# Kernel tuning notes

Hardware: AMD Instinct MI355X
Metric: run time of the kernel (lower is better)

## Reference

```python
import jax, jax.numpy as jnp
import numpy as np

B_SZ, T, D_IN, D_STATE, D_OUT = 32, 4096, 128, 128, 128


def setup_inputs() -> dict:
    key = jax.random.key(0)
    k1, k2, k3, k4, k5 = jax.random.split(key, 5)
    inputs = jax.random.normal(k1, (B_SZ, T, D_IN), dtype=jnp.float32)
    # A ~ orthogonal initializer scaled to spectral radius 0.9 for a stable recurrence
    Araw = jax.random.normal(k2, (D_STATE, D_STATE), dtype=jnp.float32)
    Q, _ = jnp.linalg.qr(Araw)
    A = 0.9 * Q
    B = jax.random.normal(k3, (D_STATE, D_IN), dtype=jnp.float32) / np.sqrt(D_IN)
    C = jax.random.normal(k4, (D_OUT, D_STATE), dtype=jnp.float32) / np.sqrt(D_STATE)
    D = jax.random.normal(k5, (D_OUT, D_IN), dtype=jnp.float32) / np.sqrt(D_IN)
    return {"inputs": inputs, "A": A, "B": B, "C": C, "D": D}


def reference(inputs, A, B, C, D):
    """x(t+1) = A x(t) + B u(t);  y(t+1) = C x(t+1) + D u(t).
    x0 = 0, return_sequences=True -> output [batch, time, d_out]."""
    x0 = jnp.zeros((inputs.shape[0], A.shape[0]), dtype=inputs.dtype)
    u_tb = jnp.swapaxes(inputs, 0, 1)  # [T, batch, d_in]

    def step(x, u):
        x1 = x @ A.T + u @ B.T          # [batch, d_state]
        y1 = x1 @ C.T + u @ D.T         # [batch, d_out]
        return x1, y1

    _, ys = jax.lax.scan(step, x0, u_tb)
    return jnp.swapaxes(ys, 0, 1)       # [batch, T, d_out]
```

## Files before the change

### kernel.cpp

```cpp
#include <hip/hip_runtime.h>
#include <cstddef>
#include <cstdint>

#define DIM 128
#define T_LEN 4096
#define BATCH 32
#define L_CH 32
#define N_CH 128
#define N_CHAINS 4096
#define KFULL 4096

typedef float f32x4 __attribute__((ext_vector_type(4)));
typedef short s16x8 __attribute__((ext_vector_type(8)));
typedef unsigned short u16x4 __attribute__((ext_vector_type(4)));
typedef unsigned short u16x8 __attribute__((ext_vector_type(8)));
typedef unsigned int u32;

#define OFF_UBF  0
#define OFF_A64  8388608
#define OFF_A96  8404992
#define OFF_A128 8421376
#define OFF_VBF  8437760
#define OFF_MCBF 8716288
#define OFF_SBF  12582912
#define OFF_KBF  12845056
#define OFF_CABF 13107200
#define OFF_WBF  13377536
#define OFF_AP   13639680
#define OFF_CA   14180352
#define OFF_K    14704640
#define OFF_W    15228928
#define OFF_B    15753216
#define OFF_C    15769600
#define OFF_D    15785984
#define AP(d)    (OFF_AP + (d) * 16384)

__device__ __forceinline__ f32x4 ld_pin(const float* p) {
    return *reinterpret_cast<const volatile f32x4*>(p);
}
__device__ __forceinline__ unsigned short f2bf(float x) {
    u32 u = __builtin_bit_cast(u32, x);
    return (unsigned short)((u + 0x7FFFu + ((u >> 16) & 1u)) >> 16);
}
__device__ __forceinline__ void gld16(const void* g, void* l) {
    __builtin_amdgcn_global_load_lds((const __attribute__((address_space(1))) u32*)g,
                                     (__attribute__((address_space(3))) u32*)l, 16, 0, 0);
}

__global__ void k_init(const float* __restrict__ u, const float* __restrict__ A,
                       const float* __restrict__ B, const float* __restrict__ C,
                       const float* __restrict__ D, float* __restrict__ wsf) {
    if (blockIdx.x < 8192) {
        unsigned short* ubf = (unsigned short*)(wsf + OFF_UBF);
        const size_t e0 = (size_t)(blockIdx.x * 256 + threadIdx.x) * 8;
        const f32x4 v0 = *reinterpret_cast<const f32x4*>(u + e0);
        const f32x4 v1 = *reinterpret_cast<const f32x4*>(u + e0 + 4);
        u16x8 o;
        o[0] = f2bf(v0.x); o[1] = f2bf(v0.y); o[2] = f2bf(v0.z); o[3] = f2bf(v0.w);
        o[4] = f2bf(v1.x); o[5] = f2bf(v1.y); o[6] = f2bf(v1.z); o[7] = f2bf(v1.w);
        *reinterpret_cast<u16x8*>(ubf + e0) = o;
    } else {
        const int e0 = ((blockIdx.x - 8192) * 256 + threadIdx.x) * 4;
        const int mat = e0 >> 14, rem = e0 & 16383;
        const float* src = (mat == 0) ? A : (mat == 1) ? B : (mat == 2) ? C : D;
        const int dst = (mat == 0) ? AP(1) : (mat == 1) ? OFF_B : (mat == 2) ? OFF_C : OFF_D;
        *reinterpret_cast<f32x4*>(wsf + dst + rem) =
            *reinterpret_cast<const f32x4*>(src + rem);
    }
}

__global__ void k_castmats(float* __restrict__ wsf) {
    const int e0 = (blockIdx.x * 256 + threadIdx.x) * 4;
    unsigned short* KBF  = (unsigned short*)(wsf + OFF_KBF);
    unsigned short* CABF = (unsigned short*)(wsf + OFF_CABF);
    unsigned short* WBF  = (unsigned short*)(wsf + OFF_WBF);
    unsigned short* MCBF = (unsigned short*)(wsf + OFF_MCBF);
    u16x4 o;
    unsigned short* dst;
    if (e0 < 524288) {
        const f32x4 v = *reinterpret_cast<const f32x4*>(wsf + OFF_K + e0);
        o[0] = f2bf(v.x); o[1] = f2bf(v.y); o[2] = f2bf(v.z); o[3] = f2bf(v.w);
        dst = KBF + e0;
    } else if (e0 < 1048576) {
        const int i2 = e0 - 524288;
        const f32x4 v = *reinterpret_cast<const f32x4*>(wsf + OFF_CA + i2);
        o[0] = f2bf(v.x); o[1] = f2bf(v.y); o[2] = f2bf(v.z); o[3] = f2bf(v.w);
        dst = CABF + 16384 + i2;
    } else if (e0 < 1572864) {
        const int widx = e0 - 1048576;
        const int i = widx >> 12, j = (widx >> 7) & 31, kp = widx & 127;
        const int srco = (j == 31) ? (OFF_B + i * 128 + kp)
                                   : (OFF_W + j * 16384 + i * 128 + kp);
        const f32x4 v = *reinterpret_cast<const f32x4*>(wsf + srco);
        o[0] = f2bf(v.x); o[1] = f2bf(v.y); o[2] = f2bf(v.z); o[3] = f2bf(v.w);
        dst = WBF + widx;
    } else {
        const int mloc = e0 - 1572864;
        const int irow = mloc / 640;
        const int rem  = mloc - irow * 640;
        const int e    = rem >> 7;
        const int k    = rem & 127;
        if (e == 0) {
#pragma unroll
            for (int j = 0; j < 4; ++j)
                o[j] = (k + j == irow) ? (unsigned short)0x3F80 : (unsigned short)0;
        } else {
            const int moff = (e == 1) ? AP(32) : (e == 2) ? OFF_A64
                           : (e == 3) ? OFF_A96 : OFF_A128;
            const f32x4 v = *reinterpret_cast<const f32x4*>(wsf + moff + irow * 128 + k);
            o[0] = f2bf(v.x); o[1] = f2bf(v.y); o[2] = f2bf(v.z); o[3] = f2bf(v.w);
        }
        dst = MCBF + mloc;
    }
    *reinterpret_cast<u16x4*>(dst) = o;
}

struct MMDesc { int n; int xo[64]; int yo[64]; int oo[64]; int ao[64]; };

__global__ __launch_bounds__(256, 1) void k_mmb(float* __restrict__ wsf, MMDesc d) {
    const int mm = blockIdx.x >> 2, sub = blockIdx.x & 3;
    const float* X = wsf + d.xo[mm];
    const float* Y = wsf + d.yo[mm];
    float* O = wsf + d.oo[mm];
    const int ao = d.ao[mm];
    __shared__ __align__(16) float Ys[DIM][DIM];
    const int t = threadIdx.x;
#pragma unroll
    for (int i = 0; i < 16; ++i) {
        const int j = t + i * 256;
        reinterpret_cast<f32x4*>(&Ys[0][0])[j] = reinterpret_cast<const f32x4*>(Y)[j];
    }
    const int r = sub * 32 + (t >> 3);
    const int c0 = (t & 7) * 16;
    f32x4 xr[32];
#pragma unroll
    for (int k = 0; k < 32; ++k) xr[k] = ld_pin(&X[r * DIM + 4 * k]);
    __syncthreads();
    float acc[16];
#pragma unroll
    for (int j = 0; j < 16; ++j) acc[j] = 0.f;
#pragma unroll
    for (int k = 0; k < DIM; ++k) {
        const float xv = ((const float*)xr)[k];
#pragma unroll
        for (int j = 0; j < 16; j += 4) {
            const f32x4 yv = *reinterpret_cast<const f32x4*>(&Ys[k][c0 + j]);
            acc[j + 0] = fmaf(xv, yv.x, acc[j + 0]);
            acc[j + 1] = fmaf(xv, yv.y, acc[j + 1]);
            acc[j + 2] = fmaf(xv, yv.z, acc[j + 2]);
            acc[j + 3] = fmaf(xv, yv.w, acc[j + 3]);
        }
    }
    if (ao >= 0) {
        const float* Ad = wsf + ao;
#pragma unroll
        for (int j = 0; j < 16; ++j) acc[j] += Ad[r * DIM + c0 + j];
    }
#pragma unroll
    for (int j = 0; j < 16; j += 4) {
        f32x4 o; o.x = acc[j]; o.y = acc[j + 1]; o.z = acc[j + 2]; o.w = acc[j + 3];
        *reinterpret_cast<f32x4*>(&O[r * DIM + c0 + j]) = o;
    }
}

__global__ __launch_bounds__(256, 2) void k_gemm1(const unsigned short* __restrict__ UBF,
                                                  const unsigned short* __restrict__ WBF,
                                                  unsigned short* __restrict__ VBF) {
    __shared__ __align__(16) unsigned short lsA[2][4096];
    __shared__ __align__(16) unsigned short lsB[2][4096];
    const int b = blockIdx.x;
    const int t = threadIdx.x, w = t >> 6, l = t & 63;
    const int wr = w >> 1, wc = w & 1;
    const int m0 = b * 128;
    const int rowA0 = w * 32 + (l >> 2);
    const int scol8 = ((l & 3) ^ ((l >> 3) & 3)) * 8;
    const int rsw   = ((l >> 4) ^ ((l >> 1) & 3)) * 8;
    const int wvb = w * 1024;
    unsigned short* Vb = VBF + b * 17408;
    {
        u16x4 z; z[0] = 0; z[1] = 0; z[2] = 0; z[3] = 0;
        *reinterpret_cast<u16x4*>(Vb + t * 4) = z;
    }
    f32x4 acc[4][4];
#pragma unroll
    for (int a = 0; a < 4; ++a)
#pragma unroll
        for (int c = 0; c < 4; ++c) acc[a][c] = (f32x4)(0.f);

#define STAGE1(q, buf) do {                                                        \
    const int kq = (q) * 32 + scol8;                                               \
    const unsigned short* ga = UBF + (size_t)(m0 + rowA0) * KFULL + kq;            \
    const unsigned short* gb = WBF + (size_t)rowA0 * KFULL + kq;                   \
    gld16(ga, &lsA[buf][wvb]);  gld16(ga + 16 * KFULL, &lsA[buf][wvb + 512]);      \
    gld16(gb, &lsB[buf][wvb]);  gld16(gb + 16 * KFULL, &lsB[buf][wvb + 512]);      \
} while (0)

    STAGE1(0, 0);
    __syncthreads();
#pragma unroll 1
    for (int q = 0; q < 128; ++q) {
        const int buf = q & 1;
        if (q + 1 < 128) STAGE1(q + 1, buf ^ 1);
        s16x8 af[4], bfr[4];
#pragma unroll
        for (int mi = 0; mi < 4; ++mi)
            af[mi] = *(const s16x8*)(&lsA[buf][(wr * 64 + mi * 16 + (l & 15)) * 32 + rsw]);
#pragma unroll
        for (int ni = 0; ni < 4; ++ni)
            bfr[ni] = *(const s16x8*)(&lsB[buf][(wc * 64 + ni * 16 + (l & 15)) * 32 + rsw]);
#pragma unroll
        for (int mi = 0; mi < 4; ++mi)
#pragma unroll
            for (int ni = 0; ni < 4; ++ni)
                acc[mi][ni] = __builtin_amdgcn_mfma_f32_16x16x32_bf16(af[mi], bfr[ni], acc[mi][ni], 0, 0, 0);
        __syncthreads();
    }
    const int row0 = wr * 64 + (l >> 4) * 4;
    const int col0 = wc * 64 + (l & 15);
#pragma unroll
    for (int mi = 0; mi < 4; ++mi)
#pragma unroll
        for (int ni = 0; ni < 4; ++ni)
#pragma unroll
            for (int jj = 0; jj < 4; ++jj)
                Vb[(8 + row0 + mi * 16 + jj) * 128 + col0 + ni * 16] = f2bf(acc[mi][ni][jj]);
#undef STAGE1
}

__global__ __launch_bounds__(256, 2) void k_comb2(const unsigned short* __restrict__ VBF,
                                                  const unsigned short* __restrict__ MCBF,
                                                  unsigned short* __restrict__ SBF) {
    __shared__ __align__(16) unsigned short lsA[2][4096];
    __shared__ __align__(16) unsigned short lsB[2][4096];
    const int b = blockIdx.x;
    const int t = threadIdx.x, w = t >> 6, l = t & 63;
    const int wr = w >> 1, wc = w & 1;
    const int rowA0 = w * 32 + (l >> 2);
    const int scol8 = ((l & 3) ^ ((l >> 3) & 3)) * 8;
    const int rsw   = ((l >> 4) ^ ((l >> 1) & 3)) * 8;
    const int wvb = w * 1024;
    const unsigned short* Vb = VBF + b * 17408;

    f32x4 acc[4][4];
#pragma unroll
    for (int a = 0; a < 4; ++a)
#pragma unroll
        for (int c = 0; c < 4; ++c) acc[a][c] = (f32x4)(0.f);

#define STAGEC(q, buf) do {                                                        \
    const int kq = (q) * 32 + scol8;                                               \
    const int e = kq >> 7, kk = kq & 127;                                          \
    const unsigned short* ga = Vb + (8 + rowA0 - 1 - e) * 128 + kk;                \
    const unsigned short* gb = MCBF + rowA0 * 640 + kq;                            \
    gld16(ga, &lsA[buf][wvb]);  gld16(ga + 16 * 128, &lsA[buf][wvb + 512]);        \
    gld16(gb, &lsB[buf][wvb]);  gld16(gb + 16 * 640, &lsB[buf][wvb + 512]);        \
} while (0)

    STAGEC(0, 0);
    __syncthreads();
#pragma unroll 1
    for (int q = 0; q < 20; ++q) {
        const int buf = q & 1;
        if (q + 1 < 20) STAGEC(q + 1, buf ^ 1);
        s16x8 af[4], bfr[4];
#pragma unroll
        for (int mi = 0; mi < 4; ++mi)
            af[mi] = *(const s16x8*)(&lsA[buf][(wr * 64 + mi * 16 + (l & 15)) * 32 + rsw]);
#pragma unroll
        for (int ni = 0; ni < 4; ++ni)
            bfr[ni] = *(const s16x8*)(&lsB[buf][(wc * 64 + ni * 16 + (l & 15)) * 32 + rsw]);
#pragma unroll
        for (int mi = 0; mi < 4; ++mi)
#pragma unroll
            for (int ni = 0; ni < 4; ++ni)
                acc[mi][ni] = __builtin_amdgcn_mfma_f32_16x16x32_bf16(af[mi], bfr[ni], acc[mi][ni], 0, 0, 0);
        __syncthreads();
    }
    const int row0 = wr * 64 + (l >> 4) * 4;
    const int col0 = wc * 64 + (l & 15);
#pragma unroll
    for (int mi = 0; mi < 4; ++mi)
#pragma unroll
        for (int ni = 0; ni < 4; ++ni)
#pragma unroll
            for (int jj = 0; jj < 4; ++jj)
                SBF[(size_t)(b * 128 + row0 + mi * 16 + jj) * 128 + col0 + ni * 16] =
                    f2bf(acc[mi][ni][jj]);
#undef STAGEC
}

__global__ __launch_bounds__(256, 2) void k_gemm3(const unsigned short* __restrict__ UBF,
                                                  const unsigned short* __restrict__ SBF,
                                                  const unsigned short* __restrict__ KBF,
                                                  const unsigned short* __restrict__ CABF,
                                                  float* __restrict__ out) {
    __shared__ __align__(16) unsigned short lsA[2][4096];
    __shared__ __align__(16) unsigned short lsB[2][4096];
    const int pp = blockIdx.x >> 5;
    const int bm = blockIdx.x & 31;
    const int t = threadIdx.x, w = t >> 6, l = t & 63;
    const int wr = w >> 1, wc = w & 1;
    const int m0 = bm * 128;
    const int rowA0 = w * 32 + (l >> 2);
    const int scol8 = ((l & 3) ^ ((l >> 3) & 3)) * 8;
    const int rsw   = ((l >> 4) ^ ((l >> 1) & 3)) * 8;
    const int wvb = w * 1024;
    const int row0 = wr * 64 + (l >> 4) * 4;
    const int col0 = wc * 64 + (l & 15);

#define STAGE3(q, buf) do {                                                            \
    const unsigned short *ga, *gb;  int strA, strB;                                    \
    if ((q) < 4 * (r + 1)) {                                                           \
        ga = UBF + (size_t)(m0 + rowA0) * KFULL + (q) * 32 + scol8;  strA = KFULL;     \
        gb = KBF + (size_t)(r - ((q) >> 2)) * 16384 + rowA0 * 128                      \
             + ((q) & 3) * 32 + scol8;                               strB = 128;       \
    } else {                                                                           \
        ga = SBF + (size_t)(m0 + rowA0) * 128 + ((q) & 3) * 32 + scol8;  strA = 128;   \
        gb = CABF + (size_t)(r + 1) * 16384 + rowA0 * 128 + ((q) & 3) * 32 + scol8;    \
        strB = 128;                                                                    \
    }                                                                                  \
    gld16(ga, &lsA[buf][wvb]);  gld16(ga + 16 * strA, &lsA[buf][wvb + 512]);           \
    gld16(gb, &lsB[buf][wvb]);  gld16(gb + 16 * strB, &lsB[buf][wvb + 512]);           \
} while (0)

#pragma unroll 1
    for (int h = 0; h < 2; ++h) {
        const int r = h ? pp : (31 - pp);
        const int NS = 4 * r + 8;
        f32x4 acc[4][4];
#pragma unroll
        for (int a = 0; a < 4; ++a)
#pragma unroll
            for (int c = 0; c < 4; ++c) acc[a][c] = (f32x4)(0.f);
        STAGE3(0, 0);
        __syncthreads();
#pragma unroll 1
        for (int q = 0; q < NS; ++q) {
            const int buf = q & 1;
            if (q + 1 < NS) STAGE3(q + 1, buf ^ 1);
            s16x8 af[4], bfr[4];
#pragma unroll
            for (int mi = 0; mi < 4; ++mi)
                af[mi] = *(const s16x8*)(&lsA[buf][(wr * 64 + mi * 16 + (l & 15)) * 32 + rsw]);
#pragma unroll
            for (int ni = 0; ni < 4; ++ni)
                bfr[ni] = *(const s16x8*)(&lsB[buf][(wc * 64 + ni * 16 + (l & 15)) * 32 + rsw]);
#pragma unroll
            for (int mi = 0; mi < 4; ++mi)
#pragma unroll
                for (int ni = 0; ni < 4; ++ni)
                    acc[mi][ni] = __builtin_amdgcn_mfma_f32_16x16x32_bf16(af[mi], bfr[ni], acc[mi][ni], 0, 0, 0);
            __syncthreads();
        }
#pragma unroll
        for (int mi = 0; mi < 4; ++mi)
#pragma unroll
            for (int ni = 0; ni < 4; ++ni)
#pragma unroll
                for (int jj = 0; jj < 4; ++jj)
                    out[(size_t)(m0 + row0 + mi * 16 + jj) * KFULL + r * 128 + col0 + ni * 16] =
                        acc[mi][ni][jj];
    }
#undef STAGE3
}

extern "C" void kernel_launch(void* const* d_in, const int* in_sizes, int n_in,
                              void* d_out, int out_size, void* d_ws, size_t ws_size,
                              hipStream_t stream) {
    const float* u  = (const float*)d_in[0];
    const float* Am = (const float*)d_in[1];
    const float* Bm = (const float*)d_in[2];
    const float* Cm = (const float*)d_in[3];
    const float* Dm = (const float*)d_in[4];
    float* out = (float*)d_out;
    float* wsf = (float*)d_ws;

    unsigned short* UBF  = (unsigned short*)(wsf + OFF_UBF);
    unsigned short* SBF  = (unsigned short*)(wsf + OFF_SBF);
    unsigned short* KBF  = (unsigned short*)(wsf + OFF_KBF);
    unsigned short* CABF = (unsigned short*)(wsf + OFF_CABF);
    unsigned short* WBF  = (unsigned short*)(wsf + OFF_WBF);
    unsigned short* VBF  = (unsigned short*)(wsf + OFF_VBF);
    unsigned short* MCBF = (unsigned short*)(wsf + OFF_MCBF);

    hipLaunchKernelGGL(k_init, dim3(8256), dim3(256), 0, stream, u, Am, Bm, Cm, Dm, wsf);

    MMDesc s;
    s.n = 1; s.xo[0] = AP(1); s.yo[0] = AP(1); s.oo[0] = AP(2); s.ao[0] = -1;
    hipLaunchKernelGGL(k_mmb, dim3(4), dim3(256), 0, stream, wsf, s);
    s.n = 2;
    s.xo[0] = AP(2); s.yo[0] = AP(1); s.oo[0] = AP(3); s.ao[0] = -1;
    s.xo[1] = AP(2); s.yo[1] = AP(2); s.oo[1] = AP(4); s.ao[1] = -1;
    hipLaunchKernelGGL(k_mmb, dim3(8), dim3(256), 0, stream, wsf, s);
    s.n = 4;
    for (int i = 0; i < 4; ++i) { s.xo[i] = AP(4); s.yo[i] = AP(1 + i); s.oo[i] = AP(5 + i); s.ao[i] = -1; }
    hipLaunchKernelGGL(k_mmb, dim3(16), dim3(256), 0, stream, wsf, s);
    s.n = 8;
    for (int i = 0; i < 8; ++i) { s.xo[i] = AP(8); s.yo[i] = AP(1 + i); s.oo[i] = AP(9 + i); s.ao[i] = -1; }
    hipLaunchKernelGGL(k_mmb, dim3(32), dim3(256), 0, stream, wsf, s);
    s.n = 16;
    for (int i = 0; i < 16; ++i) { s.xo[i] = AP(16); s.yo[i] = AP(1 + i); s.oo[i] = AP(17 + i); s.ao[i] = -1; }
    hipLaunchKernelGGL(k_mmb, dim3(64), dim3(256), 0, stream, wsf, s);
    s.n = 34;
    for (int i = 0; i < 32; ++i) { s.xo[i] = OFF_C; s.yo[i] = AP(1 + i); s.oo[i] = OFF_CA + i * 16384; s.ao[i] = -1; }
    s.xo[32] = OFF_C;  s.yo[32] = OFF_B;  s.oo[32] = OFF_K;   s.ao[32] = OFF_D;
    s.xo[33] = AP(32); s.yo[33] = AP(32); s.oo[33] = OFF_A64; s.ao[33] = -1;
    hipLaunchKernelGGL(k_mmb, dim3(136), dim3(256), 0, stream, wsf, s);
    s.n = 64;
    for (int i = 0; i < 31; ++i) { s.xo[i] = OFF_CA + i * 16384; s.yo[i] = OFF_B; s.oo[i] = OFF_K + (i + 1) * 16384; s.ao[i] = -1; }
    for (int j = 0; j < 31; ++j) { s.xo[31 + j] = AP(31 - j); s.yo[31 + j] = OFF_B; s.oo[31 + j] = OFF_W + j * 16384; s.ao[31 + j] = -1; }
    s.xo[62] = OFF_A64; s.yo[62] = AP(32);  s.oo[62] = OFF_A96;  s.ao[62] = -1;
    s.xo[63] = OFF_A64; s.yo[63] = OFF_A64; s.oo[63] = OFF_A128; s.ao[63] = -1;
    hipLaunchKernelGGL(k_mmb, dim3(256), dim3(256), 0, stream, wsf, s);

    hipLaunchKernelGGL(k_castmats, dim3(1616), dim3(256), 0, stream, wsf);
    hipLaunchKernelGGL(k_gemm1, dim3(BATCH), dim3(256), 0, stream, UBF, WBF, VBF);
    hipLaunchKernelGGL(k_comb2, dim3(BATCH), dim3(256), 0, stream, VBF, MCBF, SBF);
    hipLaunchKernelGGL(k_gemm3, dim3(512), dim3(256), 0, stream, UBF, SBF, KBF, CABF, out);
}
```

Baseline: 394.9 us.

## Split-K gemm1, fuse bf16 casts into matmul epilogue, unpair gemm3 blocks

k_gemm1 previously ran only 32 blocks over the full K=4096. It now splits K four ways across 128 blocks that write fp32 partials, and a new k_vred kernel sums the partials and writes the bf16 V buffer with its zero padding. The bf16 casts of K, CA and W move into the k_mmb epilogue through new bo/bs descriptor fields, which shrinks the cast kernel to MC and the B column. k_gemm3 drops its paired triangular loop and launches 1024 blocks, one per chunk tile, so the GPU has more blocks in flight. The cost is an extra kernel launch, the fp32 partial traffic, and worse load balance in gemm3 because tile lengths now vary.

After: 341.2 us. -13.6%, faster.

```diff
diff --git a/kernel.cpp b/kernel.cpp
--- a/kernel.cpp
+++ b/kernel.cpp
@@ -22,6 +22,7 @@
 #define OFF_A128 8421376
 #define OFF_VBF  8437760
 #define OFF_MCBF 8716288
+#define OFF_VP2  8757248
 #define OFF_SBF  12582912
 #define OFF_KBF  12845056
 #define OFF_CABF 13107200
@@ -69,35 +70,15 @@
     }
 }
 
-__global__ void k_castmats(float* __restrict__ wsf) {
+__global__ void k_castm2(float* __restrict__ wsf) {
     const int e0 = (blockIdx.x * 256 + threadIdx.x) * 4;
-    unsigned short* KBF  = (unsigned short*)(wsf + OFF_KBF);
-    unsigned short* CABF = (unsigned short*)(wsf + OFF_CABF);
+    unsigned short* MCBF = (unsigned short*)(wsf + OFF_MCBF);
     unsigned short* WBF  = (unsigned short*)(wsf + OFF_WBF);
-    unsigned short* MCBF = (unsigned short*)(wsf + OFF_MCBF);
     u16x4 o;
     unsigned short* dst;
-    if (e0 < 524288) {
-        const f32x4 v = *reinterpret_cast<const f32x4*>(wsf + OFF_K + e0);
-        o[0] = f2bf(v.x); o[1] = f2bf(v.y); o[2] = f2bf(v.z); o[3] = f2bf(v.w);
-        dst = KBF + e0;
-    } else if (e0 < 1048576) {
-        const int i2 = e0 - 524288;
-        const f32x4 v = *reinterpret_cast<const f32x4*>(wsf + OFF_CA + i2);
-        o[0] = f2bf(v.x); o[1] = f2bf(v.y); o[2] = f2bf(v.z); o[3] = f2bf(v.w);
-        dst = CABF + 16384 + i2;
-    } else if (e0 < 1572864) {
-        const int widx = e0 - 1048576;
-        const int i = widx >> 12, j = (widx >> 7) & 31, kp = widx & 127;
-        const int srco = (j == 31) ? (OFF_B + i * 128 + kp)
-                                   : (OFF_W + j * 16384 + i * 128 + kp);
-        const f32x4 v = *reinterpret_cast<const f32x4*>(wsf + srco);
-        o[0] = f2bf(v.x); o[1] = f2bf(v.y); o[2] = f2bf(v.z); o[3] = f2bf(v.w);
-        dst = WBF + widx;
-    } else {
-        const int mloc = e0 - 1572864;
-        const int irow = mloc / 640;
-        const int rem  = mloc - irow * 640;
+    if (e0 < 81920) {
+        const int irow = e0 / 640;
+        const int rem  = e0 - irow * 640;
         const int e    = rem >> 7;
         const int k    = rem & 127;
         if (e == 0) {
@@ -110,12 +91,18 @@
             const f32x4 v = *reinterpret_cast<const f32x4*>(wsf + moff + irow * 128 + k);
             o[0] = f2bf(v.x); o[1] = f2bf(v.y); o[2] = f2bf(v.z); o[3] = f2bf(v.w);
         }
-        dst = MCBF + mloc;
+        dst = MCBF + e0;
+    } else {
+        const int widx = e0 - 81920;
+        const int i = widx >> 7, k = widx & 127;
+        const f32x4 v = *reinterpret_cast<const f32x4*>(wsf + OFF_B + i * 128 + k);
+        o[0] = f2bf(v.x); o[1] = f2bf(v.y); o[2] = f2bf(v.z); o[3] = f2bf(v.w);
+        dst = WBF + i * 4096 + 3968 + k;
     }
     *reinterpret_cast<u16x4*>(dst) = o;
 }
 
-struct MMDesc { int n; int xo[64]; int yo[64]; int oo[64]; int ao[64]; };
+struct MMDesc { int n; int xo[64]; int yo[64]; int oo[64]; int ao[64]; int bo[64]; int bs[64]; };
 
 __global__ __launch_bounds__(256, 1) void k_mmb(float* __restrict__ wsf, MMDesc d) {
     const int mm = blockIdx.x >> 2, sub = blockIdx.x & 3;
@@ -161,14 +148,24 @@
         f32x4 o; o.x = acc[j]; o.y = acc[j + 1]; o.z = acc[j + 2]; o.w = acc[j + 3];
         *reinterpret_cast<f32x4*>(&O[r * DIM + c0 + j]) = o;
     }
+    if (d.bo[mm] >= 0) {
+        unsigned short* bw = (unsigned short*)wsf + (size_t)d.bo[mm] + (size_t)r * d.bs[mm] + c0;
+#pragma unroll
+        for (int j = 0; j < 16; j += 4) {
+            u16x4 ob;
+            ob[0] = f2bf(acc[j]); ob[1] = f2bf(acc[j + 1]);
+            ob[2] = f2bf(acc[j + 2]); ob[3] = f2bf(acc[j + 3]);
+            *reinterpret_cast<u16x4*>(bw + j) = ob;
+        }
+    }
 }
 
 __global__ __launch_bounds__(256, 2) void k_gemm1(const unsigned short* __restrict__ UBF,
                                                   const unsigned short* __restrict__ WBF,
-                                                  unsigned short* __restrict__ VBF) {
+                                                  float* __restrict__ VP) {
     __shared__ __align__(16) unsigned short lsA[2][4096];
     __shared__ __align__(16) unsigned short lsB[2][4096];
-    const int b = blockIdx.x;
+    const int b = blockIdx.x >> 2, ksp = blockIdx.x & 3;
     const int t = threadIdx.x, w = t >> 6, l = t & 63;
     const int wr = w >> 1, wc = w & 1;
     const int m0 = b * 128;
@@ -176,11 +173,8 @@
     const int scol8 = ((l & 3) ^ ((l >> 3) & 3)) * 8;
     const int rsw   = ((l >> 4) ^ ((l >> 1) & 3)) * 8;
     const int wvb = w * 1024;
-    unsigned short* Vb = VBF + b * 17408;
-    {
-        u16x4 z; z[0] = 0; z[1] = 0; z[2] = 0; z[3] = 0;
-        *reinterpret_cast<u16x4*>(Vb + t * 4) = z;
-    }
+    const int kb = ksp * 1024;
+
     f32x4 acc[4][4];
 #pragma unroll
     for (int a = 0; a < 4; ++a)
@@ -188,7 +182,7 @@
         for (int c = 0; c < 4; ++c) acc[a][c] = (f32x4)(0.f);
 
 #define STAGE1(q, buf) do {                                                        \
-    const int kq = (q) * 32 + scol8;                                               \
+    const int kq = kb + (q) * 32 + scol8;                                          \
     const unsigned short* ga = UBF + (size_t)(m0 + rowA0) * KFULL + kq;            \
     const unsigned short* gb = WBF + (size_t)rowA0 * KFULL + kq;                   \
     gld16(ga, &lsA[buf][wvb]);  gld16(ga + 16 * KFULL, &lsA[buf][wvb + 512]);      \
@@ -198,9 +192,9 @@
     STAGE1(0, 0);
     __syncthreads();
 #pragma unroll 1
-    for (int q = 0; q < 128; ++q) {
+    for (int q = 0; q < 32; ++q) {
         const int buf = q & 1;
-        if (q + 1 < 128) STAGE1(q + 1, buf ^ 1);
+        if (q + 1 < 32) STAGE1(q + 1, buf ^ 1);
         s16x8 af[4], bfr[4];
 #pragma unroll
         for (int mi = 0; mi < 4; ++mi)
@@ -215,6 +209,7 @@
                 acc[mi][ni] = __builtin_amdgcn_mfma_f32_16x16x32_bf16(af[mi], bfr[ni], acc[mi][ni], 0, 0, 0);
         __syncthreads();
     }
+    float* vp = VP + (size_t)ksp * (N_CHAINS * DIM);
     const int row0 = wr * 64 + (l >> 4) * 4;
     const int col0 = wc * 64 + (l & 15);
 #pragma unroll
@@ -223,8 +218,30 @@
         for (int ni = 0; ni < 4; ++ni)
 #pragma unroll
             for (int jj = 0; jj < 4; ++jj)
-                Vb[(8 + row0 + mi * 16 + jj) * 128 + col0 + ni * 16] = f2bf(acc[mi][ni][jj]);
+                vp[(size_t)(m0 + row0 + mi * 16 + jj) * DIM + col0 + ni * 16] = acc[mi][ni][jj];
 #undef STAGE1
+}
+
+__global__ void k_vred(const float* __restrict__ VP, unsigned short* __restrict__ VBF) {
+    if (blockIdx.x < 512) {
+        const int g = (blockIdx.x * 256 + threadIdx.x) * 4;
+        f32x4 s = *reinterpret_cast<const f32x4*>(VP + g);
+#pragma unroll
+        for (int sp = 1; sp < 4; ++sp) {
+            const f32x4 v = *reinterpret_cast<const f32x4*>(VP + sp * 524288 + g);
+            s.x += v.x; s.y += v.y; s.z += v.z; s.w += v.w;
+        }
+        const int m = g >> 7, i = g & 127;
+        const int b = m >> 7, c = m & 127;
+        u16x4 o;
+        o[0] = f2bf(s.x); o[1] = f2bf(s.y); o[2] = f2bf(s.z); o[3] = f2bf(s.w);
+        *reinterpret_cast<u16x4*>(VBF + b * 17408 + (8 + c) * 128 + i) = o;
+    } else {
+        const int z = ((blockIdx.x - 512) * 256 + threadIdx.x) * 4;
+        const int b = z >> 10, rem = z & 1023;
+        u16x4 zz; zz[0] = 0; zz[1] = 0; zz[2] = 0; zz[3] = 0;
+        *reinterpret_cast<u16x4*>(VBF + b * 17408 + rem) = zz;
+    }
 }
 
 __global__ __launch_bounds__(256, 2) void k_comb2(const unsigned short* __restrict__ VBF,
@@ -296,7 +313,7 @@
                                                   float* __restrict__ out) {
     __shared__ __align__(16) unsigned short lsA[2][4096];
     __shared__ __align__(16) unsigned short lsB[2][4096];
-    const int pp = blockIdx.x >> 5;
+    const int r = 31 - (blockIdx.x >> 5);
     const int bm = blockIdx.x & 31;
     const int t = threadIdx.x, w = t >> 6, l = t & 63;
     const int wr = w >> 1, wc = w & 1;
@@ -305,8 +322,13 @@
     const int scol8 = ((l & 3) ^ ((l >> 3) & 3)) * 8;
     const int rsw   = ((l >> 4) ^ ((l >> 1) & 3)) * 8;
     const int wvb = w * 1024;
-    const int row0 = wr * 64 + (l >> 4) * 4;
-    const int col0 = wc * 64 + (l & 15);
+    const int NS = 4 * r + 8;
+
+    f32x4 acc[4][4];
+#pragma unroll
+    for (int a = 0; a < 4; ++a)
+#pragma unroll
+        for (int c = 0; c < 4; ++c) acc[a][c] = (f32x4)(0.f);
 
 #define STAGE3(q, buf) do {                                                            \
     const unsigned short *ga, *gb;  int strA, strB;                                    \
@@ -323,44 +345,36 @@
     gld16(gb, &lsB[buf][wvb]);  gld16(gb + 16 * strB, &lsB[buf][wvb + 512]);           \
 } while (0)
 
+    STAGE3(0, 0);
+    __syncthreads();
 #pragma unroll 1
-    for (int h = 0; h < 2; ++h) {
-        const int r = h ? pp : (31 - pp);
-        const int NS = 4 * r + 8;
-        f32x4 acc[4][4];
-#pragma unroll
-        for (int a = 0; a < 4; ++a)
-#pragma unroll
-            for (int c = 0; c < 4; ++c) acc[a][c] = (f32x4)(0.f);
-        STAGE3(0, 0);
+    for (int q = 0; q < NS; ++q) {
+        const int buf = q & 1;
+        if (q + 1 < NS) STAGE3(q + 1, buf ^ 1);
+        s16x8 af[4], bfr[4];
+#pragma unroll
+        for (int mi = 0; mi < 4; ++mi)
+            af[mi] = *(const s16x8*)(&lsA[buf][(wr * 64 + mi * 16 + (l & 15)) * 32 + rsw]);
+#pragma unroll
+        for (int ni = 0; ni < 4; ++ni)
+            bfr[ni] = *(const s16x8*)(&lsB[buf][(wc * 64 + ni * 16 + (l & 15)) * 32 + rsw]);
+#pragma unroll
+        for (int mi = 0; mi < 4; ++mi)
+#pragma unroll
+            for (int ni = 0; ni < 4; ++ni)
+                acc[mi][ni] = __builtin_amdgcn_mfma_f32_16x16x32_bf16(af[mi], bfr[ni], acc[mi][ni], 0, 0, 0);
         __syncthreads();
-#pragma unroll 1
-        for (int q = 0; q < NS; ++q) {
-            const int buf = q & 1;
-            if (q + 1 < NS) STAGE3(q + 1, buf ^ 1);
-            s16x8 af[4], bfr[4];
-#pragma unroll
-            for (int mi = 0; mi < 4; ++mi)
-                af[mi] = *(const s16x8*)(&lsA[buf][(wr * 64 + mi * 16 + (l & 15)) * 32 + rsw]);
-#pragma unroll
-            for (int ni = 0; ni < 4; ++ni)
-                bfr[ni] = *(const s16x8*)(&lsB[buf][(wc * 64 + ni * 16 + (l & 15)) * 32 + rsw]);
-#pragma unroll
-            for (int mi = 0; mi < 4; ++mi)
-#pragma unroll
-                for (int ni = 0; ni < 4; ++ni)
-                    acc[mi][ni] = __builtin_amdgcn_mfma_f32_16x16x32_bf16(af[mi], bfr[ni], acc[mi][ni], 0, 0, 0);
-            __syncthreads();
-        }
-#pragma unroll
-        for (int mi = 0; mi < 4; ++mi)
-#pragma unroll
-            for (int ni = 0; ni < 4; ++ni)
-#pragma unroll
-                for (int jj = 0; jj < 4; ++jj)
-                    out[(size_t)(m0 + row0 + mi * 16 + jj) * KFULL + r * 128 + col0 + ni * 16] =
-                        acc[mi][ni][jj];
-    }
+    }
+    const int row0 = wr * 64 + (l >> 4) * 4;
+    const int col0 = wc * 64 + (l & 15);
+#pragma unroll
+    for (int mi = 0; mi < 4; ++mi)
+#pragma unroll
+        for (int ni = 0; ni < 4; ++ni)
+#pragma unroll
+            for (int jj = 0; jj < 4; ++jj)
+                out[(size_t)(m0 + row0 + mi * 16 + jj) * KFULL + r * 128 + col0 + ni * 16] =
+                    acc[mi][ni][jj];
 #undef STAGE3
 }
 
@@ -382,10 +396,16 @@
     unsigned short* WBF  = (unsigned short*)(wsf + OFF_WBF);
     unsigned short* VBF  = (unsigned short*)(wsf + OFF_VBF);
     unsigned short* MCBF = (unsigned short*)(wsf + OFF_MCBF);
+    float* VP2 = wsf + OFF_VP2;
+
+    const int KBF_U  = 2 * OFF_KBF;
+    const int CABF_U = 2 * OFF_CABF;
+    const int WBF_U  = 2 * OFF_WBF;
 
     hipLaunchKernelGGL(k_init, dim3(8256), dim3(256), 0, stream, u, Am, Bm, Cm, Dm, wsf);
 
     MMDesc s;
+    for (int i = 0; i < 64; ++i) { s.bo[i] = -1; s.bs[i] = 0; }
     s.n = 1; s.xo[0] = AP(1); s.yo[0] = AP(1); s.oo[0] = AP(2); s.ao[0] = -1;
     hipLaunchKernelGGL(k_mmb, dim3(4), dim3(256), 0, stream, wsf, s);
     s.n = 2;
@@ -402,19 +422,30 @@
     for (int i = 0; i < 16; ++i) { s.xo[i] = AP(16); s.yo[i] = AP(1 + i); s.oo[i] = AP(17 + i); s.ao[i] = -1; }
     hipLaunchKernelGGL(k_mmb, dim3(64), dim3(256), 0, stream, wsf, s);
     s.n = 34;
-    for (int i = 0; i < 32; ++i) { s.xo[i] = OFF_C; s.yo[i] = AP(1 + i); s.oo[i] = OFF_CA + i * 16384; s.ao[i] = -1; }
+    for (int i = 0; i < 32; ++i) {
+        s.xo[i] = OFF_C; s.yo[i] = AP(1 + i); s.oo[i] = OFF_CA + i * 16384; s.ao[i] = -1;
+        s.bo[i] = CABF_U + (i + 1) * 16384; s.bs[i] = 128;
+    }
     s.xo[32] = OFF_C;  s.yo[32] = OFF_B;  s.oo[32] = OFF_K;   s.ao[32] = OFF_D;
-    s.xo[33] = AP(32); s.yo[33] = AP(32); s.oo[33] = OFF_A64; s.ao[33] = -1;
+    s.bo[32] = KBF_U;  s.bs[32] = 128;
+    s.xo[33] = AP(32); s.yo[33] = AP(32); s.oo[33] = OFF_A64; s.ao[33] = -1; s.bo[33] = -1;
     hipLaunchKernelGGL(k_mmb, dim3(136), dim3(256), 0, stream, wsf, s);
     s.n = 64;
-    for (int i = 0; i < 31; ++i) { s.xo[i] = OFF_CA + i * 16384; s.yo[i] = OFF_B; s.oo[i] = OFF_K + (i + 1) * 16384; s.ao[i] = -1; }
-    for (int j = 0; j < 31; ++j) { s.xo[31 + j] = AP(31 - j); s.yo[31 + j] = OFF_B; s.oo[31 + j] = OFF_W + j * 16384; s.ao[31 + j] = -1; }
-    s.xo[62] = OFF_A64; s.yo[62] = AP(32);  s.oo[62] = OFF_A96;  s.ao[62] = -1;
-    s.xo[63] = OFF_A64; s.yo[63] = OFF_A64; s.oo[63] = OFF_A128; s.ao[63] = -1;
+    for (int i = 0; i < 31; ++i) {
+        s.xo[i] = OFF_CA + i * 16384; s.yo[i] = OFF_B; s.oo[i] = OFF_K + (i + 1) * 16384; s.ao[i] = -1;
+        s.bo[i] = KBF_U + (i + 1) * 16384; s.bs[i] = 128;
+    }
+    for (int j = 0; j < 31; ++j) {
+        s.xo[31 + j] = AP(31 - j); s.yo[31 + j] = OFF_B; s.oo[31 + j] = OFF_W + j * 16384; s.ao[31 + j] = -1;
+        s.bo[31 + j] = WBF_U + j * 128; s.bs[31 + j] = 4096;
+    }
+    s.xo[62] = OFF_A64; s.yo[62] = AP(32);  s.oo[62] = OFF_A96;  s.ao[62] = -1; s.bo[62] = -1;
+    s.xo[63] = OFF_A64; s.yo[63] = OFF_A64; s.oo[63] = OFF_A128; s.ao[63] = -1; s.bo[63] = -1;
     hipLaunchKernelGGL(k_mmb, dim3(256), dim3(256), 0, stream, wsf, s);
 
-    hipLaunchKernelGGL(k_castmats, dim3(1616), dim3(256), 0, stream, wsf);
-    hipLaunchKernelGGL(k_gemm1, dim3(BATCH), dim3(256), 0, stream, UBF, WBF, VBF);
+    hipLaunchKernelGGL(k_castm2, dim3(96), dim3(256), 0, stream, wsf);
+    hipLaunchKernelGGL(k_gemm1, dim3(128), dim3(256), 0, stream, UBF, WBF, VP2);
+    hipLaunchKernelGGL(k_vred, dim3(544), dim3(256), 0, stream, VP2, VBF);
     hipLaunchKernelGGL(k_comb2, dim3(BATCH), dim3(256), 0, stream, VBF, MCBF, SBF);
-    hipLaunchKernelGGL(k_gemm3, dim3(512), dim3(256), 0, stream, UBF, SBF, KBF, CABF, out);
-}
+    hipLaunchKernelGGL(k_gemm3, dim3(1024), dim3(256), 0, stream, UBF, SBF, KBF, CABF, out);
+}
```
